# Kernel tuning notes

Hardware: AMD Instinct MI355X
Metric: run time of the kernel (lower is better)

## Reference

```python
import jax, jax.numpy as jnp
import numpy as np

B, T, E, H = 4, 1024, 768, 12
D = E // H          # head_dim = 64
TEMP = 1.0          # temperature t


def setup_inputs() -> dict:
    key = jax.random.key(0)
    ks = jax.random.split(key, 19)
    inp = {}
    for i, name in enumerate(["query1", "query2", "query3", "key", "value"]):
        inp[name] = jax.random.normal(ks[i], (B, T, E), dtype=jnp.float32)
    # learned params: 6 Linear(E, E) layers (q1,q2,q3,k,v,out), torch layout W:[out,in]
    names = ["q1", "q2", "q3", "k", "v", "o"]
    for j, n in enumerate(names):
        inp[f"W{n}"] = jax.random.normal(ks[5 + 2 * j], (E, E), dtype=jnp.float32) * 0.02
        inp[f"b{n}"] = jax.random.normal(ks[6 + 2 * j], (E,), dtype=jnp.float32) * 0.02
    return inp


def _heads(x):
    # [B,T,E] -> [B,T,H,D]
    return x.reshape(B, T, H, D)


def _flat_softmax_scores(q, k):
    # q,k: [B,T,H,D]; scores: [B,H,T,T]
    s = jnp.einsum("bthd,bshd->bhts", q, k) / jnp.sqrt(jnp.float32(D))
    # global softmax over flattened T*T per (B,H), then scale by T
    s = jax.nn.softmax((s / TEMP).reshape(B, H, T * T), axis=-1)
    return s.reshape(B, H, T, T) * T


def reference(query1, query2, query3, key, value,
              Wq1, bq1, Wq2, bq2, Wq3, bq3, Wk, bk, Wv, bv, Wo, bo):
    q1 = _heads(query1 @ Wq1.T + bq1)
    q2 = _heads(query2 @ Wq2.T + bq2)
    q3 = _heads(query3 @ Wq3.T + bq3)
    k = _heads(key @ Wk.T + bk)
    v = _heads(value @ Wv.T + bv)
    a1 = _flat_softmax_scores(q1, k)
    a2 = _flat_softmax_scores(q2, k)
    a3 = _flat_softmax_scores(q3, k)
    attn = (a1 + a2 + a3) / 3.0          # [B,H,T,T]
    out = jnp.einsum("bhts,bshd->bthd", attn, v).reshape(B, T, E)
    return out @ Wo.T + bo
```

## Files before the change

kernel.cpp:

```cpp
#include <hip/hip_runtime.h>
#include <hip/hip_bf16.h>

#define Bb 4
#define Tt 1024
#define Ee 768
#define Hh 12
#define Dd 64
#define NTOK (Bb*Tt)

typedef __attribute__((ext_vector_type(8))) short bf16x8;
typedef __attribute__((ext_vector_type(4))) float f32x4;

__device__ __forceinline__ f32x4 mfma16(bf16x8 a, bf16x8 b, f32x4 c) {
  return __builtin_amdgcn_mfma_f32_16x16x32_bf16(a, b, c, 0, 0, 0);
}

__device__ __forceinline__ ushort f2b(float f) {
  uint u = __builtin_bit_cast(uint, f);
  return (ushort)((u + 0x7fffu + ((u >> 16) & 1u)) >> 16);
}
__device__ __forceinline__ uint pack2(float a, float b) {
  return (uint)f2b(a) | ((uint)f2b(b) << 16);
}

typedef const __attribute__((address_space(1))) void GV;
typedef __attribute__((address_space(3))) void LV;
__device__ __forceinline__ void gload16(const void* g, void* l) {
  __builtin_amdgcn_global_load_lds((GV*)g, (LV*)l, 16, 0, 0);
}

struct CvtSeg { const float* src; ushort* dst; int n8; };
struct CvtArgs { CvtSeg seg[11]; };

__global__ __launch_bounds__(256) void convert_kernel(CvtArgs a) {
  const CvtSeg s = a.seg[blockIdx.y];
  const int i = blockIdx.x * 256 + threadIdx.x;
  if (i >= s.n8) return;
  const float4 v0 = ((const float4*)s.src)[2*i];
  const float4 v1 = ((const float4*)s.src)[2*i + 1];
  uint4 o;
  o.x = pack2(v0.x, v0.y); o.y = pack2(v0.z, v0.w);
  o.z = pack2(v1.x, v1.y); o.w = pack2(v1.z, v1.w);
  ((uint4*)s.dst)[i] = o;
}

template<bool OUT_BF16>
__device__ __forceinline__ void gemm_bf16(
    const ushort* __restrict__ A, const ushort* __restrict__ Bw,
    const float* __restrict__ bias, void* __restrict__ Cp,
    const int K, const int N)
{
  __shared__ ushort Ash[128][64];
  __shared__ ushort Bsh[128][64];
  const int tid  = threadIdx.x;
  const int lane = tid & 63;
  const int wave = tid >> 6;
  const int m0 = blockIdx.x * 128;
  const int n0 = blockIdx.y * 128;
  const int wm = (wave >> 1) << 6;
  const int wn = (wave & 1) << 6;
  const int srow = lane >> 3;
  const int scol = ((lane & 7) ^ srow) << 3;
  const ushort* Ag = A  + (size_t)(m0 + wave*8 + srow) * K + scol;
  const ushort* Bg = Bw + (size_t)(n0 + wave*8 + srow) * K + scol;

  f32x4 acc[4][4] = {};
  for (int k0 = 0; k0 < K; k0 += 64) {
    __syncthreads();
#pragma unroll
    for (int rr = 0; rr < 4; rr++) {
      gload16(Ag + (size_t)(rr*32) * K + k0, &Ash[rr*32 + wave*8][0]);
      gload16(Bg + (size_t)(rr*32) * K + k0, &Bsh[rr*32 + wave*8][0]);
    }
    __syncthreads();
#pragma unroll
    for (int kk = 0; kk < 2; kk++) {
      const int pcb = (((lane >> 4) << 4) + kk*64) ^ ((lane & 7) << 4);
      bf16x8 af[4], bfv[4];
#pragma unroll
      for (int m = 0; m < 4; m++)
        af[m] = *(const bf16x8*)((const char*)&Ash[wm + m*16 + (lane & 15)][0] + pcb);
#pragma unroll
      for (int n = 0; n < 4; n++)
        bfv[n] = *(const bf16x8*)((const char*)&Bsh[wn + n*16 + (lane & 15)][0] + pcb);
#pragma unroll
      for (int m = 0; m < 4; m++)
#pragma unroll
        for (int n = 0; n < 4; n++)
          acc[m][n] = mfma16(af[m], bfv[n], acc[m][n]);
    }
  }
#pragma unroll
  for (int n = 0; n < 4; n++) {
    const int col = n0 + wn + n*16 + (lane & 15);
    const float bv = bias[col];
#pragma unroll
    for (int m = 0; m < 4; m++) {
#pragma unroll
      for (int r = 0; r < 4; r++) {
        const int row = m0 + wm + m*16 + ((lane >> 4) << 2) + r;
        const float v = acc[m][n][r] + bv;
        if (OUT_BF16) ((ushort*)Cp)[(size_t)row * N + col] = f2b(v);
        else          ((float*)Cp)[(size_t)row * N + col] = v;
      }
    }
  }
}

struct ProjPtrs {
  const ushort* X[5];
  const ushort* W[5];
  const float* b[5];
  ushort* out[5];
};

__global__ __launch_bounds__(256, 2) void proj5_kernel(ProjPtrs p) {
  const int z = blockIdx.z;
  gemm_bf16<true>(p.X[z], p.W[z], p.b[z], p.out[z], Ee, Ee);
}

__global__ __launch_bounds__(256, 2) void outproj_kernel(
    const ushort* __restrict__ A, const ushort* __restrict__ W,
    const float* __restrict__ bias, float* __restrict__ C) {
  gemm_bf16<false>(A, W, bias, C, Ee, Ee);
}

#define SCALE 0.125f

__global__ __launch_bounds__(256, 2) void attn_pass1(
    const ushort* __restrict__ q1, const ushort* __restrict__ q2,
    const ushort* __restrict__ q3, const ushort* __restrict__ kmat,
    float* __restrict__ Z)
{
  const int bh = blockIdx.x;
  const int b = bh / Hh, h = bh % Hh;
  const int lane = threadIdx.x & 63;
  const int wave = threadIdx.x >> 6;
  const int trow0 = blockIdx.y * 128 + wave * 32;

  __shared__ ushort Ksh[64][64];

  const int srow = lane >> 3;
  const int scolb = ((lane & 7) ^ srow) << 4;
  const ushort* Kg = kmat + (size_t)(b*Tt)*Ee + h*Dd;

  const ushort* qs[3] = {q1, q2, q3};
  bf16x8 qf[3][2][2];
#pragma unroll
  for (int j = 0; j < 3; j++)
#pragma unroll
    for (int m = 0; m < 2; m++)
#pragma unroll
      for (int kk = 0; kk < 2; kk++) {
        const int t = trow0 + m*16 + (lane & 15);
        const int d = kk*32 + ((lane >> 4) << 3);
        qf[j][m][kk] = *(const bf16x8*)(qs[j] + ((size_t)(b*Tt + t))*Ee + h*Dd + d);
      }

  float zacc[3] = {0.f, 0.f, 0.f};
  for (int s0 = 0; s0 < Tt; s0 += 64) {
    __syncthreads();
#pragma unroll
    for (int rr = 0; rr < 2; rr++) {
      const int rowbase = rr*32 + wave*8;
      gload16((const char*)(Kg + (size_t)(s0 + rowbase + srow)*Ee) + scolb,
              &Ksh[rowbase][0]);
    }
    __syncthreads();
    bf16x8 kf[4][2];
#pragma unroll
    for (int n = 0; n < 4; n++)
#pragma unroll
      for (int kk = 0; kk < 2; kk++)
        kf[n][kk] = *(const bf16x8*)((const char*)&Ksh[n*16 + (lane & 15)][0] +
                      ((((lane >> 4) << 4) + kk*64) ^ ((lane & 7) << 4)));
#pragma unroll
    for (int j = 0; j < 3; j++) {
      f32x4 sacc[2][4] = {};
#pragma unroll
      for (int kk = 0; kk < 2; kk++)
#pragma unroll
        for (int m = 0; m < 2; m++)
#pragma unroll
          for (int n = 0; n < 4; n++)
            sacc[m][n] = mfma16(qf[j][m][kk], kf[n][kk], sacc[m][n]);
      float s = 0.f;
#pragma unroll
      for (int m = 0; m < 2; m++)
#pragma unroll
        for (int n = 0; n < 4; n++)
#pragma unroll
          for (int r = 0; r < 4; r++)
            s += __expf(sacc[m][n][r] * SCALE);
      zacc[j] += s;
    }
  }
#pragma unroll
  for (int j = 0; j < 3; j++) {
    float v = zacc[j];
#pragma unroll
    for (int off = 32; off > 0; off >>= 1) v += __shfl_xor(v, off, 64);
    if (lane == 0) atomicAdd(&Z[bh*3 + j], v);
  }
}

__global__ __launch_bounds__(256, 2) void attn_pass2(
    const ushort* __restrict__ q1, const ushort* __restrict__ q2,
    const ushort* __restrict__ q3, const ushort* __restrict__ kmat,
    const ushort* __restrict__ vmat, const float* __restrict__ Z,
    ushort* __restrict__ O)
{
  const int bh = blockIdx.x;
  const int b = bh / Hh, h = bh % Hh;
  const int lane = threadIdx.x & 63;
  const int wave = threadIdx.x >> 6;
  const int trow0 = blockIdx.y * 128 + wave * 32;

  __shared__ ushort Ksh[64][64];
  __shared__ ushort Vsh[64][72];
  __shared__ ushort Psh[128][72];

  const int srow = lane >> 3;
  const int scolb = ((lane & 7) ^ srow) << 4;
  const ushort* Kg = kmat + (size_t)(b*Tt)*Ee + h*Dd;

  const ushort* qs[3] = {q1, q2, q3};
  bf16x8 qf[3][2][2];
#pragma unroll
  for (int j = 0; j < 3; j++)
#pragma unroll
    for (int m = 0; m < 2; m++)
#pragma unroll
      for (int kk = 0; kk < 2; kk++) {
        const int t = trow0 + m*16 + (lane & 15);
        const int d = kk*32 + ((lane >> 4) << 3);
        qf[j][m][kk] = *(const bf16x8*)(qs[j] + ((size_t)(b*Tt + t))*Ee + h*Dd + d);
      }

  float cj[3];
#pragma unroll
  for (int j = 0; j < 3; j++) cj[j] = (float)Tt / (3.0f * Z[bh*3 + j]);

  f32x4 oacc[2][4] = {};

  for (int s0 = 0; s0 < Tt; s0 += 64) {
    __syncthreads();
#pragma unroll
    for (int rr = 0; rr < 2; rr++) {
      const int rowbase = rr*32 + wave*8;
      gload16((const char*)(Kg + (size_t)(s0 + rowbase + srow)*Ee) + scolb,
              &Ksh[rowbase][0]);
    }
    for (int i = threadIdx.x; i < 512; i += 256) {
      const int r = i & 63;
      const int c = (i >> 6) << 3;
      bf16x8 v = *(const bf16x8*)(vmat + ((size_t)(b*Tt + s0 + r))*Ee + h*Dd + c);
#pragma unroll
      for (int u = 0; u < 8; u++) Vsh[c + u][r] = (ushort)v[u];
    }
    __syncthreads();
    bf16x8 kf[4][2];
#pragma unroll
    for (int n = 0; n < 4; n++)
#pragma unroll
      for (int kk = 0; kk < 2; kk++)
        kf[n][kk] = *(const bf16x8*)((const char*)&Ksh[n*16 + (lane & 15)][0] +
                      ((((lane >> 4) << 4) + kk*64) ^ ((lane & 7) << 4)));

    f32x4 pacc[2][4] = {};
#pragma unroll
    for (int j = 0; j < 3; j++) {
      f32x4 sacc[2][4] = {};
#pragma unroll
      for (int kk = 0; kk < 2; kk++)
#pragma unroll
        for (int m = 0; m < 2; m++)
#pragma unroll
          for (int n = 0; n < 4; n++)
            sacc[m][n] = mfma16(qf[j][m][kk], kf[n][kk], sacc[m][n]);
#pragma unroll
      for (int m = 0; m < 2; m++)
#pragma unroll
        for (int n = 0; n < 4; n++)
#pragma unroll
          for (int r = 0; r < 4; r++)
            pacc[m][n][r] += cj[j] * __expf(sacc[m][n][r] * SCALE);
    }
#pragma unroll
    for (int m = 0; m < 2; m++)
#pragma unroll
      for (int n = 0; n < 4; n++)
#pragma unroll
        for (int r = 0; r < 4; r++)
          Psh[wave*32 + m*16 + ((lane >> 4) << 2) + r][n*16 + (lane & 15)] = f2b(pacc[m][n][r]);
#pragma unroll
    for (int kk = 0; kk < 2; kk++) {
      bf16x8 pa[2], vb[4];
#pragma unroll
      for (int m = 0; m < 2; m++)
        pa[m] = *(const bf16x8*)&Psh[wave*32 + m*16 + (lane & 15)][kk*32 + ((lane >> 4) << 3)];
#pragma unroll
      for (int n = 0; n < 4; n++)
        vb[n] = *(const bf16x8*)&Vsh[n*16 + (lane & 15)][kk*32 + ((lane >> 4) << 3)];
#pragma unroll
      for (int m = 0; m < 2; m++)
#pragma unroll
        for (int n = 0; n < 4; n++)
          oacc[m][n] = mfma16(pa[m], vb[n], oacc[m][n]);
    }
  }
#pragma unroll
  for (int m = 0; m < 2; m++)
#pragma unroll
    for (int n = 0; n < 4; n++)
#pragma unroll
      for (int r = 0; r < 4; r++) {
        const int t = trow0 + m*16 + ((lane >> 4) << 2) + r;
        const int d = n*16 + (lane & 15);
        O[((size_t)(b*Tt + t))*Ee + h*Dd + d] = f2b(oacc[m][n][r]);
      }
}

extern "C" void kernel_launch(void* const* d_in, const int* in_sizes, int n_in,
                              void* d_out, int out_size, void* d_ws, size_t ws_size,
                              hipStream_t stream) {
  const float* X[5];
  for (int i = 0; i < 5; i++) X[i] = (const float*)d_in[i];
  const float* W[6];  const float* bias[6];
  for (int j = 0; j < 6; j++) {
    W[j]    = (const float*)d_in[5 + 2*j];
    bias[j] = (const float*)d_in[6 + 2*j];
  }

  char* ws = (char*)d_ws;
  const size_t segX = (size_t)NTOK * Ee * sizeof(ushort);
  const size_t segW = (size_t)Ee * Ee * sizeof(ushort);
  ushort* Xbf[5];
  for (int i = 0; i < 5; i++) Xbf[i] = (ushort*)(ws + i*segX);
  ushort* Wbf[6];
  for (int j = 0; j < 6; j++) Wbf[j] = (ushort*)(ws + 5*segX + j*segW);
  ushort* Pout[5];
  for (int i = 0; i < 5; i++) Pout[i] = (ushort*)(ws + 5*segX + 6*segW + i*segX);
  ushort* Ob = Xbf[0];
  float*  Zp = (float*)(ws + 10*segX + 6*segW);

  CvtArgs ca;
  for (int i = 0; i < 5; i++) ca.seg[i]     = {X[i], Xbf[i], NTOK*Ee/8};
  for (int j = 0; j < 6; j++) ca.seg[5 + j] = {W[j], Wbf[j], Ee*Ee/8};

  ProjPtrs pp;
  for (int i = 0; i < 5; i++) { pp.X[i] = Xbf[i]; pp.W[i] = Wbf[i]; pp.b[i] = bias[i]; pp.out[i] = Pout[i]; }

  hipMemsetAsync(Zp, 0, 48*3*sizeof(float), stream);
  convert_kernel<<<dim3(1536, 11), 256, 0, stream>>>(ca);
  proj5_kernel<<<dim3(32, 6, 5), 256, 0, stream>>>(pp);
  attn_pass1<<<dim3(48, 8), 256, 0, stream>>>(Pout[0], Pout[1], Pout[2], Pout[3], Zp);
  attn_pass2<<<dim3(48, 8), 256, 0, stream>>>(Pout[0], Pout[1], Pout[2], Pout[3], Pout[4], Zp, Ob);
  outproj_kernel<<<dim3(32, 6), 256, 0, stream>>>(Ob, Wbf[5], bias[5], (float*)d_out);
}
```

Before: 178.1 us.

## Fold softmax scale and log2e into Q weights, halve attention row tiles

Multiplies the three query projection weights and biases by 0.125*log2(e) during bf16 conversion, so the attention kernels can call a raw exp2 with no per-element multiply. It also halves the query rows per block in both attention passes, from 128 to 64, doubling the grid and raising launch-bounds occupancy. This is meant to cut exponential cost and fill more CUs, since the previous 384-block grid was small. The trade-off is that each K/V tile is reused by fewer query rows, so there is more global and LDS traffic per row. Pre-scaling the weights before bf16 rounding also slightly changes numerics.

```diff
diff --git a/kernel.cpp b/kernel.cpp
--- a/kernel.cpp
+++ b/kernel.cpp
@@ -8,11 +8,16 @@
 #define Dd 64
 #define NTOK (Bb*Tt)
 
+#define QSCALE 0.18033688f
+
 typedef __attribute__((ext_vector_type(8))) short bf16x8;
 typedef __attribute__((ext_vector_type(4))) float f32x4;
 
 __device__ __forceinline__ f32x4 mfma16(bf16x8 a, bf16x8 b, f32x4 c) {
   return __builtin_amdgcn_mfma_f32_16x16x32_bf16(a, b, c, 0, 0, 0);
+}
+__device__ __forceinline__ float exp2x(float x) {
+  return __builtin_amdgcn_exp2f(x);
 }
 
 __device__ __forceinline__ ushort f2b(float f) {
@@ -29,7 +34,7 @@
   __builtin_amdgcn_global_load_lds((GV*)g, (LV*)l, 16, 0, 0);
 }
 
-struct CvtSeg { const float* src; ushort* dst; int n8; };
+struct CvtSeg { const float* src; ushort* dst; int n8; float scale; };
 struct CvtArgs { CvtSeg seg[11]; };
 
 __global__ __launch_bounds__(256) void convert_kernel(CvtArgs a) {
@@ -39,15 +44,17 @@
   const float4 v0 = ((const float4*)s.src)[2*i];
   const float4 v1 = ((const float4*)s.src)[2*i + 1];
   uint4 o;
-  o.x = pack2(v0.x, v0.y); o.y = pack2(v0.z, v0.w);
-  o.z = pack2(v1.x, v1.y); o.w = pack2(v1.z, v1.w);
+  o.x = pack2(v0.x * s.scale, v0.y * s.scale);
+  o.y = pack2(v0.z * s.scale, v0.w * s.scale);
+  o.z = pack2(v1.x * s.scale, v1.y * s.scale);
+  o.w = pack2(v1.z * s.scale, v1.w * s.scale);
   ((uint4*)s.dst)[i] = o;
 }
 
 template<bool OUT_BF16>
 __device__ __forceinline__ void gemm_bf16(
     const ushort* __restrict__ A, const ushort* __restrict__ Bw,
-    const float* __restrict__ bias, void* __restrict__ Cp,
+    const float* __restrict__ bias, const float bscale, void* __restrict__ Cp,
     const int K, const int N)
 {
   __shared__ ushort Ash[128][64];
@@ -93,7 +100,7 @@
 #pragma unroll
   for (int n = 0; n < 4; n++) {
     const int col = n0 + wn + n*16 + (lane & 15);
-    const float bv = bias[col];
+    const float bv = bias[col] * bscale;
 #pragma unroll
     for (int m = 0; m < 4; m++) {
 #pragma unroll
@@ -111,23 +118,23 @@
   const ushort* X[5];
   const ushort* W[5];
   const float* b[5];
+  float bscale[5];
   ushort* out[5];
 };
 
 __global__ __launch_bounds__(256, 2) void proj5_kernel(ProjPtrs p) {
   const int z = blockIdx.z;
-  gemm_bf16<true>(p.X[z], p.W[z], p.b[z], p.out[z], Ee, Ee);
+  gemm_bf16<true>(p.X[z], p.W[z], p.b[z], p.bscale[z], p.out[z], Ee, Ee);
 }
 
 __global__ __launch_bounds__(256, 2) void outproj_kernel(
     const ushort* __restrict__ A, const ushort* __restrict__ W,
     const float* __restrict__ bias, float* __restrict__ C) {
-  gemm_bf16<false>(A, W, bias, C, Ee, Ee);
-}
-
-#define SCALE 0.125f
-
-__global__ __launch_bounds__(256, 2) void attn_pass1(
+  gemm_bf16<false>(A, W, bias, 1.0f, C, Ee, Ee);
+}
+
+
+__global__ __launch_bounds__(256, 4) void attn_pass1(
     const ushort* __restrict__ q1, const ushort* __restrict__ q2,
     const ushort* __restrict__ q3, const ushort* __restrict__ kmat,
     float* __restrict__ Z)
@@ -136,7 +143,7 @@
   const int b = bh / Hh, h = bh % Hh;
   const int lane = threadIdx.x & 63;
   const int wave = threadIdx.x >> 6;
-  const int trow0 = blockIdx.y * 128 + wave * 32;
+  const int trow0 = blockIdx.y * 64 + wave * 16;
 
   __shared__ ushort Ksh[64][64];
 
@@ -145,17 +152,15 @@
   const ushort* Kg = kmat + (size_t)(b*Tt)*Ee + h*Dd;
 
   const ushort* qs[3] = {q1, q2, q3};
-  bf16x8 qf[3][2][2];
+  bf16x8 qf[3][2];
 #pragma unroll
   for (int j = 0; j < 3; j++)
 #pragma unroll
-    for (int m = 0; m < 2; m++)
-#pragma unroll
-      for (int kk = 0; kk < 2; kk++) {
-        const int t = trow0 + m*16 + (lane & 15);
-        const int d = kk*32 + ((lane >> 4) << 3);
-        qf[j][m][kk] = *(const bf16x8*)(qs[j] + ((size_t)(b*Tt + t))*Ee + h*Dd + d);
-      }
+    for (int kk = 0; kk < 2; kk++) {
+      const int t = trow0 + (lane & 15);
+      const int d = kk*32 + ((lane >> 4) << 3);
+      qf[j][kk] = *(const bf16x8*)(qs[j] + ((size_t)(b*Tt + t))*Ee + h*Dd + d);
+    }
 
   float zacc[3] = {0.f, 0.f, 0.f};
   for (int s0 = 0; s0 < Tt; s0 += 64) {
@@ -176,22 +181,18 @@
                       ((((lane >> 4) << 4) + kk*64) ^ ((lane & 7) << 4)));
 #pragma unroll
     for (int j = 0; j < 3; j++) {
-      f32x4 sacc[2][4] = {};
+      f32x4 sacc[4] = {};
 #pragma unroll
       for (int kk = 0; kk < 2; kk++)
 #pragma unroll
-        for (int m = 0; m < 2; m++)
-#pragma unroll
-          for (int n = 0; n < 4; n++)
-            sacc[m][n] = mfma16(qf[j][m][kk], kf[n][kk], sacc[m][n]);
+        for (int n = 0; n < 4; n++)
+          sacc[n] = mfma16(qf[j][kk], kf[n][kk], sacc[n]);
       float s = 0.f;
 #pragma unroll
-      for (int m = 0; m < 2; m++)
-#pragma unroll
-        for (int n = 0; n < 4; n++)
-#pragma unroll
-          for (int r = 0; r < 4; r++)
-            s += __expf(sacc[m][n][r] * SCALE);
+      for (int n = 0; n < 4; n++)
+#pragma unroll
+        for (int r = 0; r < 4; r++)
+          s += exp2x(sacc[n][r]);
       zacc[j] += s;
     }
   }
@@ -204,7 +205,7 @@
   }
 }
 
-__global__ __launch_bounds__(256, 2) void attn_pass2(
+__global__ __launch_bounds__(256, 3) void attn_pass2(
     const ushort* __restrict__ q1, const ushort* __restrict__ q2,
     const ushort* __restrict__ q3, const ushort* __restrict__ kmat,
     const ushort* __restrict__ vmat, const float* __restrict__ Z,
@@ -214,34 +215,32 @@
   const int b = bh / Hh, h = bh % Hh;
   const int lane = threadIdx.x & 63;
   const int wave = threadIdx.x >> 6;
-  const int trow0 = blockIdx.y * 128 + wave * 32;
+  const int trow0 = blockIdx.y * 64 + wave * 16;
 
   __shared__ ushort Ksh[64][64];
   __shared__ ushort Vsh[64][72];
-  __shared__ ushort Psh[128][72];
+  __shared__ ushort Psh[64][72];
 
   const int srow = lane >> 3;
   const int scolb = ((lane & 7) ^ srow) << 4;
   const ushort* Kg = kmat + (size_t)(b*Tt)*Ee + h*Dd;
 
   const ushort* qs[3] = {q1, q2, q3};
-  bf16x8 qf[3][2][2];
+  bf16x8 qf[3][2];
 #pragma unroll
   for (int j = 0; j < 3; j++)
 #pragma unroll
-    for (int m = 0; m < 2; m++)
-#pragma unroll
-      for (int kk = 0; kk < 2; kk++) {
-        const int t = trow0 + m*16 + (lane & 15);
-        const int d = kk*32 + ((lane >> 4) << 3);
-        qf[j][m][kk] = *(const bf16x8*)(qs[j] + ((size_t)(b*Tt + t))*Ee + h*Dd + d);
-      }
+    for (int kk = 0; kk < 2; kk++) {
+      const int t = trow0 + (lane & 15);
+      const int d = kk*32 + ((lane >> 4) << 3);
+      qf[j][kk] = *(const bf16x8*)(qs[j] + ((size_t)(b*Tt + t))*Ee + h*Dd + d);
+    }
 
   float cj[3];
 #pragma unroll
   for (int j = 0; j < 3; j++) cj[j] = (float)Tt / (3.0f * Z[bh*3 + j]);
 
-  f32x4 oacc[2][4] = {};
+  f32x4 oacc[4] = {};
 
   for (int s0 = 0; s0 < Tt; s0 += 64) {
     __syncthreads();
@@ -267,58 +266,46 @@
         kf[n][kk] = *(const bf16x8*)((const char*)&Ksh[n*16 + (lane & 15)][0] +
                       ((((lane >> 4) << 4) + kk*64) ^ ((lane & 7) << 4)));
 
-    f32x4 pacc[2][4] = {};
+    f32x4 pacc[4] = {};
 #pragma unroll
     for (int j = 0; j < 3; j++) {
-      f32x4 sacc[2][4] = {};
+      f32x4 sacc[4] = {};
 #pragma unroll
       for (int kk = 0; kk < 2; kk++)
 #pragma unroll
-        for (int m = 0; m < 2; m++)
-#pragma unroll
-          for (int n = 0; n < 4; n++)
-            sacc[m][n] = mfma16(qf[j][m][kk], kf[n][kk], sacc[m][n]);
-#pragma unroll
-      for (int m = 0; m < 2; m++)
-#pragma unroll
         for (int n = 0; n < 4; n++)
-#pragma unroll
-          for (int r = 0; r < 4; r++)
-            pacc[m][n][r] += cj[j] * __expf(sacc[m][n][r] * SCALE);
-    }
-#pragma unroll
-    for (int m = 0; m < 2; m++)
+          sacc[n] = mfma16(qf[j][kk], kf[n][kk], sacc[n]);
 #pragma unroll
       for (int n = 0; n < 4; n++)
 #pragma unroll
         for (int r = 0; r < 4; r++)
-          Psh[wave*32 + m*16 + ((lane >> 4) << 2) + r][n*16 + (lane & 15)] = f2b(pacc[m][n][r]);
+          pacc[n][r] += cj[j] * exp2x(sacc[n][r]);
+    }
+#pragma unroll
+    for (int n = 0; n < 4; n++)
+#pragma unroll
+      for (int r = 0; r < 4; r++)
+        Psh[wave*16 + ((lane >> 4) << 2) + r][n*16 + (lane & 15)] = f2b(pacc[n][r]);
 #pragma unroll
     for (int kk = 0; kk < 2; kk++) {
-      bf16x8 pa[2], vb[4];
-#pragma unroll
-      for (int m = 0; m < 2; m++)
-        pa[m] = *(const bf16x8*)&Psh[wave*32 + m*16 + (lane & 15)][kk*32 + ((lane >> 4) << 3)];
+      bf16x8 pa, vb[4];
+      pa = *(const bf16x8*)&Psh[wave*16 + (lane & 15)][kk*32 + ((lane >> 4) << 3)];
 #pragma unroll
       for (int n = 0; n < 4; n++)
         vb[n] = *(const bf16x8*)&Vsh[n*16 + (lane & 15)][kk*32 + ((lane >> 4) << 3)];
 #pragma unroll
-      for (int m = 0; m < 2; m++)
-#pragma unroll
-        for (int n = 0; n < 4; n++)
-          oacc[m][n] = mfma16(pa[m], vb[n], oacc[m][n]);
-    }
-  }
-#pragma unroll
-  for (int m = 0; m < 2; m++)
-#pragma unroll
-    for (int n = 0; n < 4; n++)
-#pragma unroll
-      for (int r = 0; r < 4; r++) {
-        const int t = trow0 + m*16 + ((lane >> 4) << 2) + r;
-        const int d = n*16 + (lane & 15);
-        O[((size_t)(b*Tt + t))*Ee + h*Dd + d] = f2b(oacc[m][n][r]);
-      }
+      for (int n = 0; n < 4; n++)
+        oacc[n] = mfma16(pa, vb[n], oacc[n]);
+    }
+  }
+#pragma unroll
+  for (int n = 0; n < 4; n++)
+#pragma unroll
+    for (int r = 0; r < 4; r++) {
+      const int t = trow0 + ((lane >> 4) << 2) + r;
+      const int d = n*16 + (lane & 15);
+      O[((size_t)(b*Tt + t))*Ee + h*Dd + d] = f2b(oacc[n][r]);
+    }
 }
 
 extern "C" void kernel_launch(void* const* d_in, const int* in_sizes, int n_in,
@@ -345,16 +332,20 @@
   float*  Zp = (float*)(ws + 10*segX + 6*segW);
 
   CvtArgs ca;
-  for (int i = 0; i < 5; i++) ca.seg[i]     = {X[i], Xbf[i], NTOK*Ee/8};
-  for (int j = 0; j < 6; j++) ca.seg[5 + j] = {W[j], Wbf[j], Ee*Ee/8};
+  for (int i = 0; i < 5; i++) ca.seg[i]     = {X[i], Xbf[i], NTOK*Ee/8, 1.0f};
+  for (int j = 0; j < 6; j++) ca.seg[5 + j] = {W[j], Wbf[j], Ee*Ee/8,
+                                               (j < 3) ? QSCALE : 1.0f};
 
   ProjPtrs pp;
-  for (int i = 0; i < 5; i++) { pp.X[i] = Xbf[i]; pp.W[i] = Wbf[i]; pp.b[i] = bias[i]; pp.out[i] = Pout[i]; }
+  for (int i = 0; i < 5; i++) {
+    pp.X[i] = Xbf[i]; pp.W[i] = Wbf[i]; pp.b[i] = bias[i]; pp.out[i] = Pout[i];
+    pp.bscale[i] = (i < 3) ? QSCALE : 1.0f;
+  }
 
   hipMemsetAsync(Zp, 0, 48*3*sizeof(float), stream);
   convert_kernel<<<dim3(1536, 11), 256, 0, stream>>>(ca);
   proj5_kernel<<<dim3(32, 6, 5), 256, 0, stream>>>(pp);
-  attn_pass1<<<dim3(48, 8), 256, 0, stream>>>(Pout[0], Pout[1], Pout[2], Pout[3], Zp);
-  attn_pass2<<<dim3(48, 8), 256, 0, stream>>>(Pout[0], Pout[1], Pout[2], Pout[3], Pout[4], Zp, Ob);
+  attn_pass1<<<dim3(48, 16), 256, 0, stream>>>(Pout[0], Pout[1], Pout[2], Pout[3], Zp);
+  attn_pass2<<<dim3(48, 16), 256, 0, stream>>>(Pout[0], Pout[1], Pout[2], Pout[3], Pout[4], Zp, Ob);
   outproj_kernel<<<dim3(32, 6), 256, 0, stream>>>(Ob, Wbf[5], bias[5], (float*)d_out);
 }
```

Result: faster. 162.6 us (-8.7%).
